# Performance work log

Hardware: AMD Instinct MI355X
Metric: run time of the kernel (lower is better)

Reference implementation:

```python
import jax, jax.numpy as jnp
import numpy as np

B, N, D, S, ITERS = 64, 2048, 256, 8, 3
SCALE = D ** -0.5
EPS_LN = 1e-5

def _ln(x, g, b):
    m = jnp.mean(x, axis=-1, keepdims=True)
    v = jnp.var(x, axis=-1, keepdims=True)
    return (x - m) / jnp.sqrt(v + EPS_LN) * g + b

def setup_inputs() -> dict:
    key = jax.random.key(0)
    ks = jax.random.split(key, 20)
    s = D ** -0.5
    f32 = jnp.float32
    return dict(
        x=jax.random.normal(ks[0], (B, N, D), f32),
        noise=jax.random.normal(ks[1], (B, S, D), f32),
        slots_mu=jax.random.normal(ks[2], (1, 1, D), f32),
        slots_sigma=jax.random.normal(ks[3], (1, 1, D), f32),
        Wq=jax.random.normal(ks[4], (D, D), f32) * s, bq=jnp.zeros((D,), f32),
        Wk=jax.random.normal(ks[5], (D, D), f32) * s, bk=jnp.zeros((D,), f32),
        Wv=jax.random.normal(ks[6], (D, D), f32) * s, bv=jnp.zeros((D,), f32),
        W_ih=jax.random.normal(ks[7], (3 * D, D), f32) * s, b_ih=jnp.zeros((3 * D,), f32),
        W_hh=jax.random.normal(ks[8], (3 * D, D), f32) * s, b_hh=jnp.zeros((3 * D,), f32),
        W1=jax.random.normal(ks[9], (D, D), f32) * s, b1=jnp.zeros((D,), f32),
        W2=jax.random.normal(ks[10], (D, D), f32) * s, b2=jnp.zeros((D,), f32),
        g_in=jnp.ones((D,), f32), be_in=jnp.zeros((D,), f32),
        g_sl=jnp.ones((D,), f32), be_sl=jnp.zeros((D,), f32),
        g_ff=jnp.ones((D,), f32), be_ff=jnp.zeros((D,), f32),
    )

def reference(x, noise, slots_mu, slots_sigma, Wq, bq, Wk, bk, Wv, bv,
              W_ih, b_ih, W_hh, b_hh, W1, b1, W2, b2,
              g_in, be_in, g_sl, be_sl, g_ff, be_ff):
    # slot init: mu + softplus(sigma) * noise  -> [B,S,D]
    slots = slots_mu + jax.nn.softplus(slots_sigma) * noise
    xn = _ln(x, g_in, be_in)
    k = xn @ Wk.T + bk  # [B,N,D]
    v = xn @ Wv.T + bv
    for _ in range(ITERS):
        prev = slots
        q = _ln(slots, g_sl, be_sl) @ Wq.T + bq  # [B,S,D]
        logits = jnp.einsum('bsd,bnd->bsn', q, k) * SCALE
        attn = jax.nn.softmax(logits, axis=-1) + 1e-8  # softmax over inputs, as in source
        attn = attn / jnp.sum(attn, axis=-1, keepdims=True)
        updates = jnp.einsum('bsn,bnd->bsd', attn, v)
        # GRUCell(input=updates, hidden=prev); torch gate order r,z,n
        gi = updates @ W_ih.T + b_ih
        gh = prev @ W_hh.T + b_hh
        ir, iz, i_n = jnp.split(gi, 3, axis=-1)
        hr, hz, h_n = jnp.split(gh, 3, axis=-1)
        r = jax.nn.sigmoid(ir + hr)
        z = jax.nn.sigmoid(iz + hz)
        n = jnp.tanh(i_n + r * h_n)
        slots = (1.0 - z) * n + z * prev
        # residual MLP
        h = jax.nn.relu(_ln(slots, g_ff, be_ff) @ W1.T + b1)
        slots = slots + (h @ W2.T + b2)
    return slots
```

## Files before the change

kernel.cpp:

```cpp
#include <hip/hip_runtime.h>
#include <cstddef>


#define BB 64
#define NN 2048
#define DD 256
#define NCH 64
#define CHK 32
#define NITER 3
#define XPITCH 264

typedef unsigned short u16;
typedef unsigned int u32;
typedef _Float16 h2 __attribute__((ext_vector_type(2)));
typedef _Float16 h4 __attribute__((ext_vector_type(4)));

#if defined(__has_builtin)
#if __has_builtin(__builtin_amdgcn_fdot2)
#define HAS_FDOT2 1
#endif
#endif

#ifdef HAS_FDOT2
#define FDOT2(a,b,c) __builtin_amdgcn_fdot2((a),(b),(c),false)
#else
#define FDOT2(a,b,c) fmaf((float)(a).y,(float)(b).y, fmaf((float)(a).x,(float)(b).x,(c)))
#endif

__device__ __forceinline__ h2 u2h2(u32 v){ union{u32 u; h2 h;} c; c.u=v; return c.h; }
__device__ __forceinline__ float u16f(u16 v){ union{u16 u; _Float16 h;} c; c.u=v; return (float)c.h; }

__global__ __launch_bounds__(256) void kA(const float* __restrict__ noise, const float* __restrict__ mu,
                                          const float* __restrict__ sig, float* __restrict__ S,
                                          const float* __restrict__ Wq, const float* __restrict__ Wk,
                                          const float* __restrict__ bq, const float* __restrict__ Wih,
                                          const float* __restrict__ Wv, const float* __restrict__ bv,
                                          const float* __restrict__ bih,
                                          float* __restrict__ Wqk, float* __restrict__ bqk,
                                          float* __restrict__ Wihv, float* __restrict__ bihv){
  __shared__ float col[256];
  const int t = threadIdx.x;
  const int blk = blockIdx.x;
  if(blk < 256){
    col[t] = Wq[t*256 + blk];
    __syncthreads();
    float acc = 0.f;
    #pragma unroll 4
    for(int j=0;j<256;j++) acc += col[j]*Wk[j*256+t];
    Wqk[blk*256+t] = acc * 0.0625f;
  } else if(blk < 1024){
    int c = blk - 256;
    col[t] = Wih[c*256+t];
    __syncthreads();
    float acc = 0.f;
    #pragma unroll 4
    for(int j=0;j<256;j++) acc += col[j]*Wv[j*256+t];
    Wihv[(size_t)c*256+t] = acc;
  } else if(blk < 1536){
    int i = (blk-1024)*256 + t;
    float sg = sig[t];
    float sp = fmaxf(sg, 0.f) + log1pf(expf(-fabsf(sg)));
    S[i] = mu[t] + sp * noise[i];
  } else if(blk == 1536){
    float acc = 0.f;
    for(int j=0;j<256;j++) acc += bq[j]*Wk[j*256+t];
    bqk[t] = acc * 0.0625f;
  } else {
    for(int c=t;c<768;c+=256){
      float acc = 0.f;
      for(int j=0;j<256;j++) acc += Wih[c*256+j]*bv[j];
      bihv[c] = acc + bih[c];
    }
  }
}

__global__ __launch_bounds__(256) void kB(const float* __restrict__ Wihv, const float* __restrict__ Whh,
                                          const float* __restrict__ W1, const float* __restrict__ W2,
                                          float* __restrict__ WihvT, float* __restrict__ WhhT,
                                          float* __restrict__ W1T, float* __restrict__ W2T,
                                          const float* __restrict__ S0, const float* __restrict__ g_sl,
                                          const float* __restrict__ be_sl, const float* __restrict__ Wqk,
                                          const float* __restrict__ bqk, float* __restrict__ Qq){
  __shared__ float tile[64][65];
  __shared__ float lnA[8][256];
  const int blk = blockIdx.x, t = threadIdx.x;
  if(blk < 128){
    const float* src; float* dst; int R, C, tb;
    if(blk < 48){ src=Wihv; dst=WihvT; R=768; C=256; tb=blk; }
    else if(blk < 96){ src=Whh; dst=WhhT; R=768; C=256; tb=blk-48; }
    else if(blk < 112){ src=W1; dst=W1T; R=256; C=256; tb=blk-96; }
    else { src=W2; dst=W2T; R=256; C=256; tb=blk-112; }
    const int tilesC = C/64;
    const int r0 = (tb/tilesC)*64, c0 = (tb%tilesC)*64;
    const int x = t&63, y = t>>6;
    #pragma unroll
    for(int k=0;k<16;k++) tile[y*16+k][x] = src[(size_t)(r0+y*16+k)*C + c0+x];
    __syncthreads();
    #pragma unroll
    for(int k=0;k<16;k++) dst[(size_t)(c0+y*16+k)*R + r0+x] = tile[x][y*16+k];
    return;
  }
  const int w = t>>6, l = t&63;
  const int r0 = (blk-128)*8;
  #pragma unroll
  for(int rr=0; rr<2; rr++){
    int r = w*2 + rr;
    float4 v = *(const float4*)(S0 + (size_t)(r0+r)*256 + l*4);
    float s1 = v.x+v.y+v.z+v.w;
    float s2 = v.x*v.x+v.y*v.y+v.z*v.z+v.w*v.w;
    #pragma unroll
    for(int off=1; off<64; off<<=1){ s1 += __shfl_xor(s1,off); s2 += __shfl_xor(s2,off); }
    float m = s1*(1.f/256.f);
    float var = s2*(1.f/256.f) - m*m;
    float rs = rsqrtf(var + 1e-5f);
    float4 gg = *(const float4*)(g_sl + l*4);
    float4 bb = *(const float4*)(be_sl + l*4);
    float4 o;
    o.x=(v.x-m)*rs*gg.x+bb.x; o.y=(v.y-m)*rs*gg.y+bb.y;
    o.z=(v.z-m)*rs*gg.z+bb.z; o.w=(v.w-m)*rs*gg.w+bb.w;
    *(float4*)(&lnA[r][l*4]) = o;
  }
  __syncthreads();
  const int c4 = l*4;
  float acc[2][4] = {};
  #pragma unroll 2
  for(int k=0;k<256;k++){
    float4 wv = *(const float4*)(Wqk + (size_t)k*256 + c4);
    float a0 = lnA[2*w][k], a1 = lnA[2*w+1][k];
    acc[0][0]+=a0*wv.x; acc[0][1]+=a0*wv.y; acc[0][2]+=a0*wv.z; acc[0][3]+=a0*wv.w;
    acc[1][0]+=a1*wv.x; acc[1][1]+=a1*wv.y; acc[1][2]+=a1*wv.z; acc[1][3]+=a1*wv.w;
  }
  float4 bq4 = *(const float4*)(bqk + c4);
  #pragma unroll
  for(int rr=0; rr<2; rr++){
    float4 o;
    o.x=acc[rr][0]+bq4.x; o.y=acc[rr][1]+bq4.y; o.z=acc[rr][2]+bq4.z; o.w=acc[rr][3]+bq4.w;
    *(float4*)(Qq + (size_t)(r0+2*w+rr)*256 + c4) = o;
  }
}

template<int ITER0>
__global__ __launch_bounds__(512) void k_attnP(const float* __restrict__ x, const float* __restrict__ g_in,
                                               const float* __restrict__ be_in, u16* __restrict__ xn,
                                               const float* __restrict__ Qq,
                                               float* __restrict__ mP, float* __restrict__ lP,
                                               u16* __restrict__ aPh){
  __shared__ __align__(16) u16 xs[CHK*XPITCH];
  __shared__ h2 qs[8][128];
  __shared__ float plT[8][32];
  __shared__ float mS[8], lS[8];
  const int b = blockIdx.x, c = blockIdx.y, t = threadIdx.x;
  const int w = t>>6, l = t&63;

  if(ITER0){
    const size_t rowbase = (size_t)b*NN + (size_t)c*CHK;
    const float* xb = x + rowbase*DD;
    float4 gg = *(const float4*)(g_in + l*4);
    float4 bb = *(const float4*)(be_in + l*4);
    #pragma unroll
    for(int k=0;k<4;k++){
      int row = w + 8*k;
      float4 v = *(const float4*)(xb + (size_t)row*256 + l*4);
      float s1 = v.x+v.y+v.z+v.w;
      float s2 = v.x*v.x + v.y*v.y + v.z*v.z + v.w*v.w;
      #pragma unroll
      for(int off=1; off<64; off<<=1){ s1 += __shfl_xor(s1,off); s2 += __shfl_xor(s2,off); }
      float m = s1*(1.f/256.f);
      float var = s2*(1.f/256.f) - m*m;
      float rs = rsqrtf(var + 1e-5f);
      union { h4 h; uint2 u2v; } pk;
      pk.h[0] = (_Float16)((v.x-m)*rs*gg.x + bb.x);
      pk.h[1] = (_Float16)((v.y-m)*rs*gg.y + bb.y);
      pk.h[2] = (_Float16)((v.z-m)*rs*gg.z + bb.z);
      pk.h[3] = (_Float16)((v.w-m)*rs*gg.w + bb.w);
      *(uint2*)(xs + (size_t)row*XPITCH + l*4) = pk.u2v;
      *(uint2*)(xn + (rowbase+row)*DD + l*4) = pk.u2v;
    }
  } else {
    const uint4* xg4 = (const uint4*)(xn + ((size_t)b*NN + (size_t)c*CHK)*DD);
    #pragma unroll
    for(int k=0;k<2;k++){
      int idx = t + 512*k;
      int n = idx>>5, j = idx&31;
      *(uint4*)(xs + (size_t)n*XPITCH + j*8) = xg4[idx];
    }
  }
  for(int i=t; i<1024; i+=512){
    int s = i>>7, p = i&127;
    h2 hv;
    hv.x = (_Float16)Qq[b*2048 + s*256 + 2*p];
    hv.y = (_Float16)Qq[b*2048 + s*256 + 2*p + 1];
    qs[s][p] = hv;
  }
  __syncthreads();

  const int r = l & 31, hf = l >> 5;
  float hd = 0.f;
  {
    const u16* xr = xs + (size_t)r*XPITCH + hf*128;
    const h2* qp0 = &qs[w][hf*64];
    #pragma unroll
    for(int d8=0; d8<16; ++d8){
      uint4 u = *(const uint4*)(xr + d8*8);
      h2 xa=u2h2(u.x), xb2=u2h2(u.y), xc=u2h2(u.z), xd=u2h2(u.w);
      const h2* qp = qp0 + d8*4;
      hd = FDOT2(xa, qp[0], hd);
      hd = FDOT2(xb2, qp[1], hd);
      hd = FDOT2(xc, qp[2], hd);
      hd = FDOT2(xd, qp[3], hd);
    }
  }
  float lg = hd + __shfl_xor(hd, 32);
  float mx = lg;
  #pragma unroll
  for(int off=1; off<32; off<<=1) mx = fmaxf(mx, __shfl_xor(mx, off));
  float p = __expf(lg - mx);
  float sm = p;
  #pragma unroll
  for(int off=1; off<32; off<<=1) sm += __shfl_xor(sm, off);
  if(l < 32) plT[w][r] = p;
  if(l == 0){ mS[w] = mx; lS[w] = sm; }
  __syncthreads();

  const size_t pb = (size_t)(b*NCH + c)*8;
  {
    float4 a4 = {0.f,0.f,0.f,0.f};
    const u16* xq = xs + 4*l;
    #pragma unroll 8
    for(int nn=0; nn<CHK; ++nn){
      uint2 u = *(const uint2*)(xq + (size_t)nn*XPITCH);
      h2 ha=u2h2(u.x), hb=u2h2(u.y);
      float pp = plT[w][nn];
      a4.x += pp*(float)ha.x; a4.y += pp*(float)ha.y;
      a4.z += pp*(float)hb.x; a4.w += pp*(float)hb.y;
    }
    union { h4 h; uint2 u2v; } pk;
    pk.h[0]=(_Float16)a4.x; pk.h[1]=(_Float16)a4.y;
    pk.h[2]=(_Float16)a4.z; pk.h[3]=(_Float16)a4.w;
    *(uint2*)(aPh + (pb + w)*256 + l*4) = pk.u2v;
  }
  if(t<8){ mP[pb+t] = mS[t]; lP[pb+t] = lS[t]; }
}

union PostU {
  float Gt[2][4][768];
  struct { float Row[4][256]; float Ht[4][256]; float Lq[4][256]; } m;
};

__global__ __launch_bounds__(512) void k_post(const float* __restrict__ mP, const float* __restrict__ lP,
                                              const u16* __restrict__ aPh, const float* __restrict__ WihvT,
                                              const float* __restrict__ bihv, const float* __restrict__ WhhT,
                                              const float* __restrict__ bhh, const float* __restrict__ Sc,
                                              const float* __restrict__ g_ff, const float* __restrict__ be_ff,
                                              const float* __restrict__ W1T, const float* __restrict__ b1,
                                              const float* __restrict__ W2T, const float* __restrict__ b2,
                                              const float* __restrict__ g_sl, const float* __restrict__ be_sl,
                                              const float* __restrict__ Wqk, const float* __restrict__ bqk,
                                              float* __restrict__ Sout, float* __restrict__ Qq, int writeQ){
  __shared__ float Ut[4][256];
  __shared__ float Sp[4][256];
  __shared__ float Hp[2][4][256];
  __shared__ PostU uu;
  __shared__ float red2[4][2];
  const int t = threadIdx.x;
  const int r0 = blockIdx.x*4;
  const int b = r0>>3;
  const int w = t>>6, l = t&63;
  const int c = t&255, hh = t>>8;

  #pragma unroll
  for(int k=0;k<2;k++){
    int idx = t + 512*k;
    int r = idx>>8, cc = idx&255;
    int rr = r0 + r, ss = rr&7;
    const float* mpb = mP + b*(NCH*8) + ss;
    const float* lpb = lP + b*(NCH*8) + ss;
    float M = -1e30f;
    #pragma unroll 8
    for(int c8=0;c8<NCH;c8++) M = fmaxf(M, mpb[c8*8]);
    float L = 0.f, u = 0.f;
    size_t base = ((size_t)b*(NCH*8) + ss)*256 + cc;
    #pragma unroll 8
    for(int c8=0;c8<NCH;c8++){
      float wgt = __expf(mpb[c8*8] - M);
      L += lpb[c8*8]*wgt;
      u += wgt*u16f(aPh[base + (size_t)c8*2048]);
    }
    Ut[r][cc] = u/L;
    Sp[r][cc] = Sc[(size_t)rr*256 + cc];
  }
  __syncthreads();

  if(t < 384){
    const int mat = t/192, q4 = (t - mat*192)*4;
    const float* WT = mat ? WhhT : WihvT;
    const float* bb2 = mat ? bhh : bihv;
    const float (*A)[256] = mat ? Sp : Ut;
    float4 bias4 = *(const float4*)(bb2 + q4);
    float4 ac0 = bias4, ac1 = bias4, ac2 = bias4, ac3 = bias4;
    const float* wp = WT + q4;
    #pragma unroll 4
    for(int d=0; d<256; ++d){
      float4 wv = *(const float4*)(wp + (size_t)d*768);
      float a0=A[0][d], a1=A[1][d], a2=A[2][d], a3=A[3][d];
      ac0.x += a0*wv.x; ac0.y += a0*wv.y; ac0.z += a0*wv.z; ac0.w += a0*wv.w;
      ac1.x += a1*wv.x; ac1.y += a1*wv.y; ac1.z += a1*wv.z; ac1.w += a1*wv.w;
      ac2.x += a2*wv.x; ac2.y += a2*wv.y; ac2.z += a2*wv.z; ac2.w += a2*wv.w;
      ac3.x += a3*wv.x; ac3.y += a3*wv.y; ac3.z += a3*wv.z; ac3.w += a3*wv.w;
    }
    *(float4*)(&uu.Gt[mat][0][q4]) = ac0;
    *(float4*)(&uu.Gt[mat][1][q4]) = ac1;
    *(float4*)(&uu.Gt[mat][2][q4]) = ac2;
    *(float4*)(&uu.Gt[mat][3][q4]) = ac3;
  }
  __syncthreads();

  #pragma unroll
  for(int k=0;k<2;k++){
    int idx = t + 512*k;
    int r = idx>>8, cc = idx&255;
    float gir = uu.Gt[0][r][cc], giz = uu.Gt[0][r][256+cc], gin = uu.Gt[0][r][512+cc];
    float ghr = uu.Gt[1][r][cc], ghz = uu.Gt[1][r][256+cc], ghn = uu.Gt[1][r][512+cc];
    float rr2 = 1.f/(1.f + __expf(-(gir+ghr)));
    float zz = 1.f/(1.f + __expf(-(giz+ghz)));
    float nn = tanhf(gin + rr2*ghn);
    Ut[r][cc] = (1.f-zz)*nn + zz*Sp[r][cc];
  }
  __syncthreads();

  if(w < 4){
    float s1=0.f, s2=0.f;
    #pragma unroll
    for(int k2=0;k2<4;k2++){ float v = Ut[w][l + 64*k2]; s1 += v; s2 += v*v; }
    #pragma unroll
    for(int off=1; off<64; off<<=1){ s1 += __shfl_xor(s1,off); s2 += __shfl_xor(s2,off); }
    if(l==0){
      float m = s1*(1.f/256.f);
      float var = s2*(1.f/256.f) - m*m;
      red2[w][0] = m; red2[w][1] = rsqrtf(var + 1e-5f);
    }
  }
  __syncthreads();
  #pragma unroll
  for(int k=0;k<2;k++){
    int idx = t + 512*k;
    int r = idx>>8, cc = idx&255;
    uu.m.Row[r][cc] = (Ut[r][cc]-red2[r][0])*red2[r][1]*g_ff[cc] + be_ff[cc];
  }
  __syncthreads();

  {
    const float* w1 = W1T + (size_t)hh*128*256 + c;
    float a0 = hh ? 0.f : b1[c], a1=a0, a2=a0, a3=a0;
    const int dB = hh*128;
    #pragma unroll 8
    for(int d=0; d<128; ++d){
      float wv = w1[(size_t)d*256];
      a0 += uu.m.Row[0][dB+d]*wv;
      a1 += uu.m.Row[1][dB+d]*wv;
      a2 += uu.m.Row[2][dB+d]*wv;
      a3 += uu.m.Row[3][dB+d]*wv;
    }
    Hp[hh][0][c]=a0; Hp[hh][1][c]=a1; Hp[hh][2][c]=a2; Hp[hh][3][c]=a3;
  }
  __syncthreads();
  #pragma unroll
  for(int k=0;k<2;k++){
    int idx = t + 512*k;
    int r = idx>>8, cc = idx&255;
    uu.m.Ht[r][cc] = fmaxf(Hp[0][r][cc]+Hp[1][r][cc], 0.f);
  }
  __syncthreads();

  {
    const float* w2 = W2T + (size_t)hh*128*256 + c;
    float a0 = hh ? 0.f : b2[c], a1=a0, a2=a0, a3=a0;
    const int dB = hh*128;
    #pragma unroll 8
    for(int d=0; d<128; ++d){
      float wv = w2[(size_t)d*256];
      a0 += uu.m.Ht[0][dB+d]*wv;
      a1 += uu.m.Ht[1][dB+d]*wv;
      a2 += uu.m.Ht[2][dB+d]*wv;
      a3 += uu.m.Ht[3][dB+d]*wv;
    }
    Hp[hh][0][c]=a0; Hp[hh][1][c]=a1; Hp[hh][2][c]=a2; Hp[hh][3][c]=a3;
  }
  __syncthreads();
  if(t < 256){
    #pragma unroll
    for(int r=0;r<4;r++){
      float sn = Hp[0][r][c] + Hp[1][r][c] + Ut[r][c];
      Sout[(size_t)(r0+r)*256 + c] = sn;
      Ut[r][c] = sn;
    }
  }

  if(writeQ){
    __syncthreads();
    if(w < 4){
      float s1=0.f, s2=0.f;
      #pragma unroll
      for(int k2=0;k2<4;k2++){ float v = Ut[w][l + 64*k2]; s1 += v; s2 += v*v; }
      #pragma unroll
      for(int off=1; off<64; off<<=1){ s1 += __shfl_xor(s1,off); s2 += __shfl_xor(s2,off); }
      if(l==0){
        float m = s1*(1.f/256.f);
        float var = s2*(1.f/256.f) - m*m;
        red2[w][0] = m; red2[w][1] = rsqrtf(var + 1e-5f);
      }
    }
    __syncthreads();
    #pragma unroll
    for(int k=0;k<2;k++){
      int idx = t + 512*k;
      int r = idx>>8, cc = idx&255;
      uu.m.Lq[r][cc] = (Ut[r][cc]-red2[r][0])*red2[r][1]*g_sl[cc] + be_sl[cc];
    }
    __syncthreads();
    {
      const float* wq = Wqk + (size_t)hh*128*256 + c;
      float a0 = hh ? 0.f : bqk[c], a1=a0, a2=a0, a3=a0;
      const int dB = hh*128;
      #pragma unroll 8
      for(int d=0; d<128; ++d){
        float wv = wq[(size_t)d*256];
        a0 += uu.m.Lq[0][dB+d]*wv;
        a1 += uu.m.Lq[1][dB+d]*wv;
        a2 += uu.m.Lq[2][dB+d]*wv;
        a3 += uu.m.Lq[3][dB+d]*wv;
      }
      Hp[hh][0][c]=a0; Hp[hh][1][c]=a1; Hp[hh][2][c]=a2; Hp[hh][3][c]=a3;
    }
    __syncthreads();
    if(t < 256){
      #pragma unroll
      for(int r=0;r<4;r++)
        Qq[(size_t)(r0+r)*256 + c] = Hp[0][r][c] + Hp[1][r][c];
    }
  }
}

extern "C" void kernel_launch(void* const* d_in, const int* in_sizes, int n_in,
                              void* d_out, int out_size, void* d_ws, size_t ws_size,
                              hipStream_t stream){
  const float* x    = (const float*)d_in[0];
  const float* noise= (const float*)d_in[1];
  const float* mu   = (const float*)d_in[2];
  const float* sig  = (const float*)d_in[3];
  const float* Wq   = (const float*)d_in[4];
  const float* bq   = (const float*)d_in[5];
  const float* Wk   = (const float*)d_in[6];
  const float* Wv   = (const float*)d_in[8];
  const float* bv   = (const float*)d_in[9];
  const float* W_ih = (const float*)d_in[10];
  const float* b_ih = (const float*)d_in[11];
  const float* W_hh = (const float*)d_in[12];
  const float* b_hh = (const float*)d_in[13];
  const float* W1m  = (const float*)d_in[14];
  const float* b1v  = (const float*)d_in[15];
  const float* W2m  = (const float*)d_in[16];
  const float* b2v  = (const float*)d_in[17];
  const float* g_in = (const float*)d_in[18];
  const float* be_in= (const float*)d_in[19];
  const float* g_sl = (const float*)d_in[20];
  const float* be_sl= (const float*)d_in[21];
  const float* g_ff = (const float*)d_in[22];
  const float* be_ff= (const float*)d_in[23];

  char* p = (char*)d_ws;
  auto alloc = [&](size_t bytes)->char*{ char* q = p; p += (bytes + 255) & ~(size_t)255; return q; };
  u16*   xn    = (u16*)  alloc((size_t)BB*NN*DD*2);
  float* Wqk   = (float*)alloc(256*256*4);
  float* bqk   = (float*)alloc(256*4);
  float* Wihv  = (float*)alloc((size_t)768*256*4);
  float* WihvT = (float*)alloc((size_t)256*768*4);
  float* bihv  = (float*)alloc(768*4);
  float* WhhT  = (float*)alloc((size_t)256*768*4);
  float* W1T   = (float*)alloc(256*256*4);
  float* W2T   = (float*)alloc(256*256*4);
  float* S0    = (float*)alloc(512*256*4);
  float* S1    = (float*)alloc(512*256*4);
  float* Qq    = (float*)alloc(512*256*4);
  float* mP    = (float*)alloc(64*NCH*8*4);
  float* lP    = (float*)alloc(64*NCH*8*4);
  u16*   aPh   = (u16*)  alloc((size_t)64*NCH*8*256*2);
  if((size_t)(p - (char*)d_ws) > ws_size) return;

  kA<<<1538, 256, 0, stream>>>(noise, mu, sig, S0, Wq, Wk, bq, W_ih, Wv, bv, b_ih,
                               Wqk, bqk, Wihv, bihv);
  kB<<<192, 256, 0, stream>>>(Wihv, W_hh, W1m, W2m, WihvT, WhhT, W1T, W2T,
                              S0, g_sl, be_sl, Wqk, bqk, Qq);

  float* Sin = S0;
  float* Sping[2] = { S1, S0 };
  for(int it=0; it<NITER; ++it){
    float* Sout = (it==NITER-1) ? (float*)d_out : Sping[it&1];
    if(it == 0)
      k_attnP<1><<<dim3(64, NCH), 512, 0, stream>>>(x, g_in, be_in, xn, Qq, mP, lP, aPh);
    else
      k_attnP<0><<<dim3(64, NCH), 512, 0, stream>>>(x, g_in, be_in, xn, Qq, mP, lP, aPh);
    k_post<<<128, 512, 0, stream>>>(mP, lP, aPh, WihvT, bihv, WhhT, b_hh, Sin, g_ff, be_ff,
                                    W1T, b1v, W2T, b2v, g_sl, be_sl, Wqk, bqk,
                                    Sout, Qq, (it<NITER-1) ? 1 : 0);
    Sin = Sout;
  }
}
```

Measured before the change: 363.2 us.

## Double attention chunk size, store Q in fp16, reorder grid to chunk-major

Chunks per batch drop from 64 to 32 and each chunk grows from 32 to 64 rows. Each lane now computes a full 256-dim dot product for one row, so the cross-half shuffle goes away and the softmax reductions span all 64 lanes. Q is produced and stored in fp16 by kB and k_post, which halves its traffic and removes the per-block float-to-half conversion. The grid is swapped so chunk index is blockIdx.x, and the k_post partial-merge work and aPh traffic shrink because there are half as many partials. The trade-off is fewer blocks (2048 vs 4096) and a serial 256-long dot chain per lane.

After: 328.3 us. 9.6% less time.

```diff
diff --git a/kernel.cpp b/kernel.cpp
--- a/kernel.cpp
+++ b/kernel.cpp
@@ -5,8 +5,8 @@
 #define BB 64
 #define NN 2048
 #define DD 256
-#define NCH 64
-#define CHK 32
+#define NCH 32
+#define CHK 64
 #define NITER 3
 #define XPITCH 264
 
@@ -29,6 +29,9 @@
 
 __device__ __forceinline__ h2 u2h2(u32 v){ union{u32 u; h2 h;} c; c.u=v; return c.h; }
 __device__ __forceinline__ float u16f(u16 v){ union{u16 u; _Float16 h;} c; c.u=v; return (float)c.h; }
+__device__ __forceinline__ u32 packh2(float a, float b){
+  union{u32 u; h2 h;} c; c.h.x=(_Float16)a; c.h.y=(_Float16)b; return c.u;
+}
 
 __global__ __launch_bounds__(256) void kA(const float* __restrict__ noise, const float* __restrict__ mu,
                                           const float* __restrict__ sig, float* __restrict__ S,
@@ -80,7 +83,7 @@
                                           float* __restrict__ W1T, float* __restrict__ W2T,
                                           const float* __restrict__ S0, const float* __restrict__ g_sl,
                                           const float* __restrict__ be_sl, const float* __restrict__ Wqk,
-                                          const float* __restrict__ bqk, float* __restrict__ Qq){
+                                          const float* __restrict__ bqk, u16* __restrict__ Qh){
   __shared__ float tile[64][65];
   __shared__ float lnA[8][256];
   const int blk = blockIdx.x, t = threadIdx.x;
@@ -133,23 +136,24 @@
   float4 bq4 = *(const float4*)(bqk + c4);
   #pragma unroll
   for(int rr=0; rr<2; rr++){
-    float4 o;
-    o.x=acc[rr][0]+bq4.x; o.y=acc[rr][1]+bq4.y; o.z=acc[rr][2]+bq4.z; o.w=acc[rr][3]+bq4.w;
-    *(float4*)(Qq + (size_t)(r0+2*w+rr)*256 + c4) = o;
+    uint2 o;
+    o.x = packh2(acc[rr][0]+bq4.x, acc[rr][1]+bq4.y);
+    o.y = packh2(acc[rr][2]+bq4.z, acc[rr][3]+bq4.w);
+    *(uint2*)(Qh + (size_t)(r0+2*w+rr)*256 + l*4) = o;
   }
 }
 
 template<int ITER0>
 __global__ __launch_bounds__(512) void k_attnP(const float* __restrict__ x, const float* __restrict__ g_in,
                                                const float* __restrict__ be_in, u16* __restrict__ xn,
-                                               const float* __restrict__ Qq,
+                                               const u16* __restrict__ Qh,
                                                float* __restrict__ mP, float* __restrict__ lP,
                                                u16* __restrict__ aPh){
   __shared__ __align__(16) u16 xs[CHK*XPITCH];
   __shared__ h2 qs[8][128];
-  __shared__ float plT[8][32];
+  __shared__ float plT[8][64];
   __shared__ float mS[8], lS[8];
-  const int b = blockIdx.x, c = blockIdx.y, t = threadIdx.x;
+  const int c = blockIdx.x, b = blockIdx.y, t = threadIdx.x;
   const int w = t>>6, l = t&63;
 
   if(ITER0){
@@ -158,7 +162,7 @@
     float4 gg = *(const float4*)(g_in + l*4);
     float4 bb = *(const float4*)(be_in + l*4);
     #pragma unroll
-    for(int k=0;k<4;k++){
+    for(int k=0;k<8;k++){
       int row = w + 8*k;
       float4 v = *(const float4*)(xb + (size_t)row*256 + l*4);
       float s1 = v.x+v.y+v.z+v.w;
@@ -168,58 +172,51 @@
       float m = s1*(1.f/256.f);
       float var = s2*(1.f/256.f) - m*m;
       float rs = rsqrtf(var + 1e-5f);
-      union { h4 h; uint2 u2v; } pk;
-      pk.h[0] = (_Float16)((v.x-m)*rs*gg.x + bb.x);
-      pk.h[1] = (_Float16)((v.y-m)*rs*gg.y + bb.y);
-      pk.h[2] = (_Float16)((v.z-m)*rs*gg.z + bb.z);
-      pk.h[3] = (_Float16)((v.w-m)*rs*gg.w + bb.w);
-      *(uint2*)(xs + (size_t)row*XPITCH + l*4) = pk.u2v;
-      *(uint2*)(xn + (rowbase+row)*DD + l*4) = pk.u2v;
+      uint2 pk;
+      pk.x = packh2((v.x-m)*rs*gg.x + bb.x, (v.y-m)*rs*gg.y + bb.y);
+      pk.y = packh2((v.z-m)*rs*gg.z + bb.z, (v.w-m)*rs*gg.w + bb.w);
+      *(uint2*)(xs + (size_t)row*XPITCH + l*4) = pk;
+      *(uint2*)(xn + (rowbase+row)*DD + l*4) = pk;
     }
   } else {
     const uint4* xg4 = (const uint4*)(xn + ((size_t)b*NN + (size_t)c*CHK)*DD);
     #pragma unroll
-    for(int k=0;k<2;k++){
+    for(int k=0;k<4;k++){
       int idx = t + 512*k;
       int n = idx>>5, j = idx&31;
       *(uint4*)(xs + (size_t)n*XPITCH + j*8) = xg4[idx];
     }
   }
-  for(int i=t; i<1024; i+=512){
-    int s = i>>7, p = i&127;
-    h2 hv;
-    hv.x = (_Float16)Qq[b*2048 + s*256 + 2*p];
-    hv.y = (_Float16)Qq[b*2048 + s*256 + 2*p + 1];
-    qs[s][p] = hv;
-  }
-  __syncthreads();
-
-  const int r = l & 31, hf = l >> 5;
-  float hd = 0.f;
   {
-    const u16* xr = xs + (size_t)r*XPITCH + hf*128;
-    const h2* qp0 = &qs[w][hf*64];
-    #pragma unroll
-    for(int d8=0; d8<16; ++d8){
+    int s = t>>6, pp = t&63;
+    uint2 v = *(const uint2*)(Qh + (size_t)(b*8+s)*256 + pp*4);
+    *(uint2*)(&qs[s][pp*2]) = v;
+  }
+  __syncthreads();
+
+  float lg = 0.f;
+  {
+    const u16* xr = xs + (size_t)l*XPITCH;
+    #pragma unroll 4
+    for(int d8=0; d8<32; ++d8){
       uint4 u = *(const uint4*)(xr + d8*8);
       h2 xa=u2h2(u.x), xb2=u2h2(u.y), xc=u2h2(u.z), xd=u2h2(u.w);
-      const h2* qp = qp0 + d8*4;
-      hd = FDOT2(xa, qp[0], hd);
-      hd = FDOT2(xb2, qp[1], hd);
-      hd = FDOT2(xc, qp[2], hd);
-      hd = FDOT2(xd, qp[3], hd);
-    }
-  }
-  float lg = hd + __shfl_xor(hd, 32);
+      const h2* qp = &qs[w][d8*4];
+      lg = FDOT2(xa, qp[0], lg);
+      lg = FDOT2(xb2, qp[1], lg);
+      lg = FDOT2(xc, qp[2], lg);
+      lg = FDOT2(xd, qp[3], lg);
+    }
+  }
   float mx = lg;
   #pragma unroll
-  for(int off=1; off<32; off<<=1) mx = fmaxf(mx, __shfl_xor(mx, off));
+  for(int off=1; off<64; off<<=1) mx = fmaxf(mx, __shfl_xor(mx, off));
   float p = __expf(lg - mx);
   float sm = p;
   #pragma unroll
-  for(int off=1; off<32; off<<=1) sm += __shfl_xor(sm, off);
-  if(l < 32) plT[w][r] = p;
-  if(l == 0){ mS[w] = mx; lS[w] = sm; }
+  for(int off=1; off<64; off<<=1) sm += __shfl_xor(sm, off);
+  plT[w][l] = p;
+  if(l==0){ mS[w] = mx; lS[w] = sm; }
   __syncthreads();
 
   const size_t pb = (size_t)(b*NCH + c)*8;
@@ -234,10 +231,10 @@
       a4.x += pp*(float)ha.x; a4.y += pp*(float)ha.y;
       a4.z += pp*(float)hb.x; a4.w += pp*(float)hb.y;
     }
-    union { h4 h; uint2 u2v; } pk;
-    pk.h[0]=(_Float16)a4.x; pk.h[1]=(_Float16)a4.y;
-    pk.h[2]=(_Float16)a4.z; pk.h[3]=(_Float16)a4.w;
-    *(uint2*)(aPh + (pb + w)*256 + l*4) = pk.u2v;
+    uint2 pk;
+    pk.x = packh2(a4.x, a4.y);
+    pk.y = packh2(a4.z, a4.w);
+    *(uint2*)(aPh + (pb + w)*256 + l*4) = pk;
   }
   if(t<8){ mP[pb+t] = mS[t]; lP[pb+t] = lS[t]; }
 }
@@ -256,7 +253,7 @@
                                               const float* __restrict__ W2T, const float* __restrict__ b2,
                                               const float* __restrict__ g_sl, const float* __restrict__ be_sl,
                                               const float* __restrict__ Wqk, const float* __restrict__ bqk,
-                                              float* __restrict__ Sout, float* __restrict__ Qq, int writeQ){
+                                              float* __restrict__ Sout, u16* __restrict__ Qh, int writeQ){
   __shared__ float Ut[4][256];
   __shared__ float Sp[4][256];
   __shared__ float Hp[2][4][256];
@@ -436,7 +433,13 @@
     if(t < 256){
       #pragma unroll
       for(int r=0;r<4;r++)
-        Qq[(size_t)(r0+r)*256 + c] = Hp[0][r][c] + Hp[1][r][c];
+        uu.m.Row[r][c] = Hp[0][r][c] + Hp[1][r][c];
+    }
+    __syncthreads();
+    {
+      int r = t>>7, pp = t&127;
+      u32 v = packh2(uu.m.Row[r][2*pp], uu.m.Row[r][2*pp+1]);
+      *(u32*)(Qh + (size_t)(r0+r)*256 + pp*2) = v;
     }
   }
 }
@@ -481,7 +484,7 @@
   float* W2T   = (float*)alloc(256*256*4);
   float* S0    = (float*)alloc(512*256*4);
   float* S1    = (float*)alloc(512*256*4);
-  float* Qq    = (float*)alloc(512*256*4);
+  u16*   Qh    = (u16*)  alloc(512*256*2);
   float* mP    = (float*)alloc(64*NCH*8*4);
   float* lP    = (float*)alloc(64*NCH*8*4);
   u16*   aPh   = (u16*)  alloc((size_t)64*NCH*8*256*2);
@@ -490,19 +493,19 @@
   kA<<<1538, 256, 0, stream>>>(noise, mu, sig, S0, Wq, Wk, bq, W_ih, Wv, bv, b_ih,
                                Wqk, bqk, Wihv, bihv);
   kB<<<192, 256, 0, stream>>>(Wihv, W_hh, W1m, W2m, WihvT, WhhT, W1T, W2T,
-                              S0, g_sl, be_sl, Wqk, bqk, Qq);
+                              S0, g_sl, be_sl, Wqk, bqk, Qh);
 
   float* Sin = S0;
   float* Sping[2] = { S1, S0 };
   for(int it=0; it<NITER; ++it){
     float* Sout = (it==NITER-1) ? (float*)d_out : Sping[it&1];
     if(it == 0)
-      k_attnP<1><<<dim3(64, NCH), 512, 0, stream>>>(x, g_in, be_in, xn, Qq, mP, lP, aPh);
+      k_attnP<1><<<dim3(NCH, 64), 512, 0, stream>>>(x, g_in, be_in, xn, Qh, mP, lP, aPh);
     else
-      k_attnP<0><<<dim3(64, NCH), 512, 0, stream>>>(x, g_in, be_in, xn, Qq, mP, lP, aPh);
+      k_attnP<0><<<dim3(NCH, 64), 512, 0, stream>>>(x, g_in, be_in, xn, Qh, mP, lP, aPh);
     k_post<<<128, 512, 0, stream>>>(mP, lP, aPh, WihvT, bihv, WhhT, b_hh, Sin, g_ff, be_ff,
                                     W1T, b1v, W2T, b2v, g_sl, be_sl, Wqk, bqk,
-                                    Sout, Qq, (it<NITER-1) ? 1 : 0);
+                                    Sout, Qh, (it<NITER-1) ? 1 : 0);
     Sin = Sout;
   }
 }
```
